# Performance work log

Hardware: AMD Instinct MI355X
Metric: run time of the kernel (lower is better)

The kernel has to match this reference:

```python
import jax, jax.numpy as jnp
import numpy as np
import math

H, D_MODEL, D_C, D_ROPE = 16, 2048, 512, 64
D_HEAD = D_MODEL // H  # 128
D_QK = D_HEAD + D_ROPE  # 192


def precompute_freqs_cis(d_rope, seq_len, base=10000.0):
    # standard RoPE frequencies over pairs -> (seq_len, d_rope//2)
    inv_freq = 1.0 / (base ** (jnp.arange(0, d_rope, 2, dtype=jnp.float32) / d_rope))
    t = jnp.arange(seq_len, dtype=jnp.float32)
    ang = jnp.outer(t, inv_freq)
    return jnp.cos(ang), jnp.sin(ang)


def apply_rotary_emb(x, cos, sin):
    # x: (..., T, d_rope); cos/sin broadcastable (..., T, d_rope//2); interleaved pairs
    x1 = x[..., 0::2]
    x2 = x[..., 1::2]
    r1 = x1 * cos - x2 * sin
    r2 = x1 * sin + x2 * cos
    return jnp.stack([r1, r2], axis=-1).reshape(x.shape)


def setup_inputs() -> dict:
    key = jax.random.key(0)
    ks = jax.random.split(key, 10)
    B, T = 2, 2048
    s = 0.02
    return {
        "query": jax.random.normal(ks[0], (B, T, D_MODEL), jnp.float32),
        "key": jax.random.normal(ks[1], (B, T, D_MODEL), jnp.float32),
        "value": jax.random.normal(ks[2], (B, T, D_MODEL), jnp.float32),
        # weights stored (in_dim, out_dim)
        "W_DKV": jax.random.normal(ks[3], (D_MODEL, D_C), jnp.float32) * s,
        "W_UK": jax.random.normal(ks[4], (D_C, H * D_HEAD), jnp.float32) * s,
        "W_UV": jax.random.normal(ks[5], (D_C, H * D_HEAD), jnp.float32) * s,
        "W_Q": jax.random.normal(ks[6], (D_MODEL, H * D_HEAD), jnp.float32) * s,
        "W_KR": jax.random.normal(ks[7], (D_MODEL, D_ROPE), jnp.float32) * s,
        "W_QR": jax.random.normal(ks[8], (D_MODEL, H * D_ROPE), jnp.float32) * s,
        "W_O": jax.random.normal(ks[9], (H * D_HEAD, D_MODEL), jnp.float32) * s,
    }


def reference(query, key, value, W_DKV, W_UK, W_UV, W_Q, W_KR, W_QR, W_O):
    B, T_q, _ = query.shape
    T_k = key.shape[1]
    # low-rank latent KV compression
    c_kv = key @ W_DKV                                   # (B, Tk, d_c)
    k_nope = (c_kv @ W_UK).reshape(B, T_k, H, D_HEAD).transpose(0, 2, 1, 3)  # bhkd
    v = (c_kv @ W_UV).reshape(B, T_k, H, D_HEAD).transpose(0, 2, 1, 3)       # bhkd
    q_nope = (query @ W_Q).reshape(B, T_q, H, D_HEAD).transpose(0, 2, 1, 3)  # bhqd
    # decoupled RoPE subspace
    k_rope_in = (key @ W_KR)[:, None, :, :]              # (B,1,Tk,d_rope) shared across heads
    q_rope_in = (query @ W_QR).reshape(B, T_q, H, D_ROPE).transpose(0, 2, 1, 3)
    cos_q, sin_q = precompute_freqs_cis(D_ROPE, T_q)
    cos_k, sin_k = precompute_freqs_cis(D_ROPE, T_k)
    q_rope = apply_rotary_emb(q_rope_in, cos_q[None, None], sin_q[None, None])
    k_rope = apply_rotary_emb(k_rope_in, cos_k[None, None], sin_k[None, None])
    k_rope = jnp.broadcast_to(k_rope, (B, H, T_k, D_ROPE))
    # concat content + rope parts
    q = jnp.concatenate([q_nope, q_rope], axis=-1)       # (B,H,Tq,d_qk)
    k = jnp.concatenate([k_nope, k_rope], axis=-1)       # (B,H,Tk,d_qk)
    scores = jnp.einsum('bhqd,bhkd->bhqk', q, k) / math.sqrt(D_QK)
    p_attn = jax.nn.softmax(scores, axis=-1)             # dropout is identity (eval/p=0)
    x = jnp.einsum('bhqk,bhkd->bhqd', p_attn, v)
    x = x.transpose(0, 2, 1, 3).reshape(B, T_q, H * D_HEAD)
    output = x @ W_O
    return output, p_attn
```

## Files before the change

kernel.cpp:

```cpp
#include <hip/hip_runtime.h>
#include <hip/hip_bf16.h>
#include <math.h>

constexpr int B_   = 2;
constexpr int T_   = 2048;
constexpr int DM   = 2048;
constexpr int H_   = 16;
constexpr int DH   = 128;
constexpr int DC   = 512;
constexpr int DR   = 64;
constexpr int DQK  = DH + DR;
constexpr int BT   = B_ * T_;
constexpr int ZBH  = B_ * H_;

typedef __bf16 bf16x8 __attribute__((ext_vector_type(8)));
typedef float  f32x4  __attribute__((ext_vector_type(4)));
typedef unsigned int u32x2 __attribute__((ext_vector_type(2)));
typedef unsigned short u16x4 __attribute__((ext_vector_type(4)));

__device__ __forceinline__ unsigned pk2(float a, float b) {
  __hip_bfloat162 t = __float22bfloat162_rn(make_float2(a, b));
  return *reinterpret_cast<unsigned*>(&t);
}
__device__ __forceinline__ unsigned short bfbits(float v) {
  __hip_bfloat16 t = __float2bfloat16(v);
  return *reinterpret_cast<unsigned short*>(&t);
}

#define WAITVM(N)   asm volatile("s_waitcnt vmcnt(" #N ")" ::: "memory")
#define BARSB() do { __builtin_amdgcn_s_barrier(); __builtin_amdgcn_sched_barrier(0); } while (0)
#define AS1 __attribute__((address_space(1)))
#define AS3 __attribute__((address_space(3)))

__global__ __launch_bounds__(256)
void prep(const float* __restrict__ query, const float* __restrict__ key,
          const float* __restrict__ W_Q, const float* __restrict__ W_QR,
          const float* __restrict__ W_DKV, const float* __restrict__ W_KR,
          const float* __restrict__ W_UK, const float* __restrict__ W_UV,
          const float* __restrict__ W_O,
          __hip_bfloat16* __restrict__ qB, __hip_bfloat16* __restrict__ kB,
          __hip_bfloat16* __restrict__ Wtqall, __hip_bfloat16* __restrict__ Wtkall,
          __hip_bfloat16* __restrict__ Wtkvup, __hip_bfloat16* __restrict__ WtO,
          float* __restrict__ ctab, float* __restrict__ stab) {
  __shared__ float tile[32][33];
  const int blk = blockIdx.x;
  const int tid = threadIdx.x;

  if (blk < 4096) {
    const float* src = (blk < 2048) ? query : key;
    __hip_bfloat16* dst = (blk < 2048) ? qB : kB;
    const long base = (long)(blk & 2047) * 4096;
    #pragma unroll
    for (int c = 0; c < 4; ++c) {
      const long off = base + c * 1024 + tid * 4;
      float4 f = *(const float4*)(src + off);
      u16x4 pk;
      pk[0] = bfbits(f.x); pk[1] = bfbits(f.y); pk[2] = bfbits(f.z); pk[3] = bfbits(f.w);
      *(u16x4*)(dst + off) = pk;
    }
    return;
  }

  int b = blk - 4096;
  const float* W = nullptr; __hip_bfloat16* Wt = nullptr; int K = 2048, N = 2048;
  if (b < 4096)               { W = W_Q;   Wt = Wtqall; }
  else if ((b -= 4096) < 2048){ W = W_QR;  Wt = Wtqall + (size_t)2048 * 2048; N = 1024; }
  else if ((b -= 2048) < 1024){ W = W_DKV; Wt = Wtkall; N = 512; }
  else if ((b -= 1024) < 128) { W = W_KR;  Wt = Wtkall + (size_t)512 * 2048; N = 64; }
  else if ((b -= 128) < 1024) { W = W_UK;  Wt = Wtkvup; K = 512; }
  else if ((b -= 1024) < 1024){ W = W_UV;  Wt = Wtkvup + (size_t)2048 * 512; K = 512; }
  else if ((b -= 1024) < 4096){ W = W_O;   Wt = WtO; }
  else if ((b -= 4096) < 192) {
    float4 z = {0.f, 0.f, 0.f, 0.f};
    *(float4*)((char*)(Wtkall + (size_t)(576 + b) * 2048) + tid * 16) = z;
    return;
  }
  else {
    b -= 192;
    const int i = b * 256 + tid;
    const int t = i >> 5, j = i & 31;
    double inv = pow(10000.0, -(double)j / 32.0);
    double ang = (double)t * inv;
    ctab[i] = (float)cos(ang);
    stab[i] = (float)sin(ang);
    return;
  }
  const int nx = N >> 5;
  const int n0 = (b % nx) << 5, k0 = (b / nx) << 5;
  const int tx = tid & 31, ty = tid >> 5;
  for (int i = ty; i < 32; i += 8)
    tile[i][tx] = W[(long)(k0 + i) * N + n0 + tx];
  __syncthreads();
  for (int i = ty; i < 32; i += 8)
    Wt[(long)(n0 + i) * K + k0 + tx] = __float2bfloat16(tile[tx][i]);
}

template <int MODE>
__global__ __launch_bounds__(256, 2)
void gemm_4w(const __hip_bfloat16* __restrict__ A, const __hip_bfloat16* __restrict__ Bt,
             void* __restrict__ C0, void* __restrict__ C1,
             int M, int N, int K, int lda,
             const float* __restrict__ ctab, const float* __restrict__ stab) {
  const int gnx = N >> 8;
  const int nwg = (M >> 7) * gnx;
  const int cpx = nwg >> 3;
  const int bid = blockIdx.x;
  const int swz = (bid & 7) * cpx + (bid >> 3);
  const int n0 = (swz % gnx) << 8;
  const int m0 = (swz / gnx) << 7;

  __shared__ __align__(16) char lds[73728];

  const int tid  = threadIdx.x;
  const int wc   = tid >> 6;
  const int lane = tid & 63;
  const int rr   = lane & 15;
  const int kq   = lane >> 4;

  const int cs16 = (((tid & 3) ^ ((tid >> 3) & 3)) << 4);
  const int srow = tid >> 2;

  auto stage = [&](int buf, int k0) {
    char* base = lds + buf * 24576;
    #pragma unroll
    for (int c = 0; c < 2; ++c) {
      const char* src = (const char*)A + (((long)(m0 + c * 64 + srow)) * lda + k0) * 2 + cs16;
      __builtin_amdgcn_global_load_lds((const AS1 void*)src,
          (AS3 void*)(base + c * 4096 + tid * 16), 16, 0, 0);
    }
    #pragma unroll
    for (int c = 0; c < 4; ++c) {
      const char* src = (const char*)Bt + (((long)(n0 + c * 64 + srow)) * K + k0) * 2 + cs16;
      __builtin_amdgcn_global_load_lds((const AS1 void*)src,
          (AS3 void*)(base + 8192 + c * 4096 + tid * 16), 16, 0, 0);
    }
  };

  const int g16 = ((kq ^ ((rr >> 1) & 3)) << 4);
  const int aoff0 = rr * 64 + g16;
  const int boff0 = 8192 + (wc * 64 + rr) * 64 + g16;

  f32x4 acc[8][4] = {};

  auto phase = [&](int buf) {
    char* base = lds + buf * 24576;
    bf16x8 a[8], b[4];
    #pragma unroll
    for (int mf = 0; mf < 8; ++mf) a[mf] = *(const bf16x8*)(base + aoff0 + mf * 1024);
    #pragma unroll
    for (int nf = 0; nf < 4; ++nf) b[nf] = *(const bf16x8*)(base + boff0 + nf * 1024);
    __builtin_amdgcn_s_setprio(1);
    #pragma unroll
    for (int mf = 0; mf < 8; ++mf)
      #pragma unroll
      for (int nf = 0; nf < 4; ++nf)
        acc[mf][nf] = __builtin_amdgcn_mfma_f32_16x16x32_bf16(a[mf], b[nf], acc[mf][nf], 0, 0, 0);
    __builtin_amdgcn_s_setprio(0);
  };

  const int NT = K >> 5;
  stage(0, 0); stage(1, 32);
  int cur = 0;
  for (int t = 0; t < NT; ++t) {
    if (t + 2 < NT)       WAITVM(6);
    else if (t + 1 < NT)  WAITVM(6);
    else                  WAITVM(0);
    BARSB();
    if (t + 2 < NT) {
      const int b2 = (cur + 2 >= 3) ? cur - 1 : cur + 2;
      stage(b2, (t + 2) << 5);
    }
    phase(cur);
    cur = (cur + 1 >= 3) ? 0 : cur + 1;
  }

  #pragma unroll
  for (int mf = 0; mf < 8; ++mf) {
    #pragma unroll
    for (int nf = 0; nf < 4; ++nf) {
      const int col = n0 + wc * 64 + nf * 16 + rr;
      const int rbase = m0 + mf * 16 + kq * 4;
      if constexpr (MODE == 1) {
        float* C = (float*)C0;
        #pragma unroll
        for (int j = 0; j < 4; ++j)
          __builtin_nontemporal_store(acc[mf][nf][j], &C[(long)(rbase + j) * N + col]);
      } else if constexpr (MODE == 2) {
        __hip_bfloat16* qall = (__hip_bfloat16*)C0;
        if (col < 2048) {
          #pragma unroll
          for (int j = 0; j < 4; ++j)
            qall[(long)(rbase + j) * 3072 + col] = __float2bfloat16(acc[mf][nf][j]);
        } else {
          const int dr = (col - 2048) & 63;
          const int jj = dr >> 1;
          #pragma unroll
          for (int j = 0; j < 4; ++j) {
            const int row = rbase + j;
            const int t = row & (T_ - 1);
            const float c = ctab[t * 32 + jj], s = stab[t * 32 + jj];
            const float v  = acc[mf][nf][j];
            const float pv = __shfl_xor(v, 1);
            const float res = (dr & 1) ? (pv * s + v * c) : (v * c - pv * s);
            qall[(long)row * 3072 + col] = __float2bfloat16(res);
          }
        }
      } else if constexpr (MODE == 4) {
        __hip_bfloat16* knope = (__hip_bfloat16*)C0;
        __hip_bfloat16* vT    = (__hip_bfloat16*)C1;
        if (col < 2048) {
          #pragma unroll
          for (int j = 0; j < 4; ++j)
            knope[(long)(rbase + j) * 2048 + col] = __float2bfloat16(acc[mf][nf][j]);
        } else {
          const int h = (col - 2048) >> 7, d = (col - 2048) & 127;
          const int z = (rbase >> 11) * 16 + h;
          const int t0 = rbase & (T_ - 1);
          u16x4 pk;
          #pragma unroll
          for (int j = 0; j < 4; ++j) pk[j] = bfbits(acc[mf][nf][j]);
          *(u16x4*)((__hip_bfloat16*)vT + ((long)z * DH + d) * T_ + t0) = pk;
        }
      }
    }
  }
}

template <int MODE>
__global__ __launch_bounds__(512, 2)
void gemm_8w(const __hip_bfloat16* __restrict__ A, const __hip_bfloat16* __restrict__ Bt,
             void* __restrict__ C0, void* __restrict__ C1,
             int M, int N, int K, int lda,
             const float* __restrict__ ctab, const float* __restrict__ stab) {
  const int gnx = N >> 8;
  const int nwg = (M >> 7) * gnx;
  const int cpx = nwg >> 3;
  const int bid = blockIdx.x;
  const int swz = (bid & 7) * cpx + (bid >> 3);
  const int n0 = (swz % gnx) << 8;
  const int m0 = (swz / gnx) << 7;

  __shared__ __align__(16) char lds[147456];

  const int tid  = threadIdx.x;
  const int wv   = tid >> 6;
  const int lane = tid & 63;
  const int wr   = wv >> 2;
  const int wc   = wv & 3;
  const int rr   = lane & 15;
  const int kq   = lane >> 4;

  const int cs16 = (((tid & 3) ^ ((tid >> 3) & 3)) << 4);
  const long arow  = m0 + (tid >> 2);
  const long brow0 = n0 + (tid >> 2);
  const long brow1 = n0 + 128 + (tid >> 2);

  auto stage = [&](int buf, int kh, int k0) {
    char* base = lds + buf * 49152 + kh * 24576;
    const long kk = (long)k0 + kh * 32;
    const char* asrc = (const char*)A + (arow * lda + kk) * 2 + cs16;
    __builtin_amdgcn_global_load_lds((const AS1 void*)asrc,
                                     (AS3 void*)(base + tid * 16), 16, 0, 0);
    const char* bsrc0 = (const char*)Bt + (brow0 * K + kk) * 2 + cs16;
    __builtin_amdgcn_global_load_lds((const AS1 void*)bsrc0,
                                     (AS3 void*)(base + 8192 + tid * 16), 16, 0, 0);
    const char* bsrc1 = (const char*)Bt + (brow1 * K + kk) * 2 + cs16;
    __builtin_amdgcn_global_load_lds((const AS1 void*)bsrc1,
                                     (AS3 void*)(base + 16384 + tid * 16), 16, 0, 0);
  };

  const int g16 = ((kq ^ ((rr >> 1) & 3)) << 4);
  const int aoff0 = (wr * 64 + rr) * 64 + g16;
  const int boff0 = 8192 + (wc * 64 + rr) * 64 + g16;

  f32x4 acc[4][4] = {};

  auto phase = [&](int buf, int kh) {
    char* base = lds + buf * 49152 + kh * 24576;
    bf16x8 a[4], b[4];
    #pragma unroll
    for (int mf = 0; mf < 4; ++mf) a[mf] = *(const bf16x8*)(base + aoff0 + mf * 1024);
    #pragma unroll
    for (int nf = 0; nf < 4; ++nf) b[nf] = *(const bf16x8*)(base + boff0 + nf * 1024);
    __builtin_amdgcn_s_setprio(1);
    #pragma unroll
    for (int mf = 0; mf < 4; ++mf)
      #pragma unroll
      for (int nf = 0; nf < 4; ++nf)
        acc[mf][nf] = __builtin_amdgcn_mfma_f32_16x16x32_bf16(a[mf], b[nf], acc[mf][nf], 0, 0, 0);
    __builtin_amdgcn_s_setprio(0);
  };

  const int NT = K >> 6;
  stage(0, 0, 0); stage(0, 1, 0);
  stage(1, 0, 64); stage(1, 1, 64);
  int cur = 0;
  for (int t = 0; t < NT; ++t) {
    const int b2 = (cur + 2 >= 3) ? cur - 1 : cur + 2;
    if (t + 2 < NT) {
      const int k2 = (t + 2) << 6;
      WAITVM(9);  BARSB();
      stage(b2, 0, k2);
      phase(cur, 0);
      WAITVM(9);  BARSB();
      stage(b2, 1, k2);
      phase(cur, 1);
    } else if (t + 2 == NT) {
      WAITVM(9);  BARSB();  phase(cur, 0);
      WAITVM(6);  BARSB();  phase(cur, 1);
    } else {
      WAITVM(3);  BARSB();  phase(cur, 0);
      WAITVM(0);  BARSB();  phase(cur, 1);
    }
    cur = (cur + 1 >= 3) ? 0 : cur + 1;
  }

  #pragma unroll
  for (int mf = 0; mf < 4; ++mf) {
    #pragma unroll
    for (int nf = 0; nf < 4; ++nf) {
      const int col = n0 + wc * 64 + nf * 16 + rr;
      const int rbase = m0 + wr * 64 + mf * 16 + kq * 4;
      if constexpr (MODE == 3) {
        __hip_bfloat16* ckv = (__hip_bfloat16*)C0;
        __hip_bfloat16* krp = (__hip_bfloat16*)C1;
        if (col < 512) {
          #pragma unroll
          for (int j = 0; j < 4; ++j)
            ckv[(long)(rbase + j) * 512 + col] = __float2bfloat16(acc[mf][nf][j]);
        } else if (col < 576) {
          const int dr = col - 512;
          const int jj = dr >> 1;
          #pragma unroll
          for (int j = 0; j < 4; ++j) {
            const int row = rbase + j;
            const int t = row & (T_ - 1);
            const float c = ctab[t * 32 + jj], s = stab[t * 32 + jj];
            const float v  = acc[mf][nf][j];
            const float pv = __shfl_xor(v, 1);
            const float res = (dr & 1) ? (pv * s + v * c) : (v * c - pv * s);
            krp[(long)row * 64 + dr] = __float2bfloat16(res);
          }
        }
      }
    }
  }
}

__global__ __launch_bounds__(512)
void fused_attn(const __hip_bfloat16* __restrict__ q_all,
                const __hip_bfloat16* __restrict__ knope,
                const __hip_bfloat16* __restrict__ kroper,
                const __hip_bfloat16* __restrict__ vTg,
                float* __restrict__ patt,
                __hip_bfloat16* __restrict__ xplain) {
  constexpr int KT = 64;
  constexpr int NKT = T_ / KT;
  const int bid = blockIdx.x;
  const int swz = (bid & 7) * 64 + (bid >> 3);
  const int z  = swz >> 4;
  const int q0 = (swz & 15) << 7;
  const int b  = z >> 4, h = z & 15;
  const int tid  = threadIdx.x;
  const int wv   = tid >> 6;
  const int lane = tid & 63;
  const int rr   = lane & 15;
  const int kq   = lane >> 4;
  const float scl = 0.0721687836487032f;

  __shared__ __align__(16) char smem[98304];
  char* const lP = smem + 81920;

  const long qrow = (long)(b * T_) + q0 + wv * 16 + rr;
  const __hip_bfloat16* qn = q_all + qrow * 3072 + h * 128;
  const __hip_bfloat16* qr = q_all + qrow * 3072 + 2048 + h * 64;
  bf16x8 qa[6];
  #pragma unroll
  for (int kc = 0; kc < 4; ++kc) qa[kc] = *(const bf16x8*)(qn + kc * 32 + kq * 8);
  #pragma unroll
  for (int kc = 0; kc < 2; ++kc) qa[4 + kc] = *(const bf16x8*)(qr + kc * 32 + kq * 8);

  auto stage_k = [&](char* dst, int kt0) {
    #pragma unroll
    for (int it = 0; it < 3; ++it) {
      const int off = it * 8192 + wv * 1024;
      const int lb  = off + lane * 16;
      const int row = lb / 384, cb = lb % 384;
      const int scb = cb ^ ((row & 7) << 4);
      const long trow = (long)(b * T_) + kt0 + row;
      const char* src = (scb < 256)
          ? (const char*)knope + trow * 4096 + h * 256 + scb
          : (const char*)kroper + trow * 128 + (scb - 256);
      __builtin_amdgcn_global_load_lds((const AS1 void*)src,
          (AS3 void*)(dst + off), 16, 0, 0);
    }
  };
  auto stage_v = [&](char* dst, int kt0) {
    #pragma unroll
    for (int it = 0; it < 2; ++it) {
      const int off = it * 8192 + wv * 1024;
      const int lb  = off + lane * 16;
      const int row = lb >> 7, cb = lb & 127;
      const int scb = cb ^ ((row & 7) << 4);
      const char* src = (const char*)vTg + ((long)(z * DH + row) * T_ + kt0) * 2 + scb;
      __builtin_amdgcn_global_load_lds((const AS1 void*)src,
          (AS3 void*)(dst + off), 16, 0, 0);
    }
  };

  auto qkt = [&](const char* kb0, f32x4 (&sacc)[4]) {
    __builtin_amdgcn_s_setprio(1);
    #pragma unroll
    for (int kc = 0; kc < 6; ++kc) {
      #pragma unroll
      for (int n = 0; n < 4; ++n) {
        const int krow = n * 16 + rr;
        bf16x8 kb = *(const bf16x8*)(kb0 + krow * 384 +
                                     ((kc * 64 + kq * 16) ^ ((krow & 7) << 4)));
        sacc[n] = __builtin_amdgcn_mfma_f32_16x16x32_bf16(kb, qa[kc], sacc[n], 0, 0, 0);
      }
    }
    __builtin_amdgcn_s_setprio(0);
  };

  float srun = 0.f;

  stage_k(smem, 0);
  stage_k(smem + 24576, KT);
  for (int kt = 0; kt < NKT; ++kt) {
    if (kt + 2 < NKT)      { stage_k(smem + ((kt + 2) & 3) * 24576, (kt + 2) * KT); WAITVM(6); }
    else if (kt + 2 == NKT) WAITVM(3);
    else                    WAITVM(0);
    BARSB();
    f32x4 sacc[4] = {};
    qkt(smem + (kt & 3) * 24576, sacc);
    float ts = 0.f;
    #pragma unroll
    for (int n = 0; n < 4; ++n)
      #pragma unroll
      for (int r = 0; r < 4; ++r) ts += __expf(sacc[n][r] * scl);
    ts += __shfl_xor(ts, 16);
    ts += __shfl_xor(ts, 32);
    srun += ts;
  }
  const float pis = 1.f / srun;

  stage_k(smem, 0);
  stage_v(smem + 49152, 0);
  BARSB();

  f32x4 oacc[8] = {};
  const int prow = wv * 16 + rr;
  int cur = 0;
  for (int kt = 0; kt < NKT; ++kt) {
    if (kt == 0) WAITVM(0); else WAITVM(4);
    BARSB();
    if (kt + 1 < NKT) {
      stage_k(smem + (cur ? 0 : 24576), (kt + 1) * KT);
      stage_v(smem + 49152 + (cur ? 0 : 16384), (kt + 1) * KT);
    }
    const char* lK = smem + (cur ? 24576 : 0);
    const char* lV = smem + 49152 + (cur ? 16384 : 0);
    f32x4 sacc[4] = {};
    qkt(lK, sacc);
    const int kt0 = kt * KT;
    #pragma unroll
    for (int n = 0; n < 4; ++n) {
      f32x4 pv;
      #pragma unroll
      for (int r = 0; r < 4; ++r) pv[r] = __expf(sacc[n][r] * scl) * pis;
      __builtin_nontemporal_store(pv,
          (f32x4*)(patt + ((long)z * T_ + q0 + prow) * T_ + kt0 + n * 16 + kq * 4));
      u32x2 pw; pw[0] = pk2(pv[0], pv[1]); pw[1] = pk2(pv[2], pv[3]);
      *(u32x2*)(lP + prow * 128 + ((n * 32 + kq * 8) ^ ((prow & 7) << 4))) = pw;
    }
    bf16x8 pa[2];
    #pragma unroll
    for (int kc = 0; kc < 2; ++kc)
      pa[kc] = *(const bf16x8*)(lP + prow * 128 + ((kc * 64 + kq * 16) ^ ((prow & 7) << 4)));
    __builtin_amdgcn_s_setprio(1);
    #pragma unroll
    for (int kc = 0; kc < 2; ++kc) {
      #pragma unroll
      for (int n = 0; n < 8; ++n) {
        const int vrow = n * 16 + rr;
        bf16x8 vb = *(const bf16x8*)(lV + vrow * 128 + ((kc * 64 + kq * 16) ^ ((vrow & 7) << 4)));
        oacc[n] = __builtin_amdgcn_mfma_f32_16x16x32_bf16(pa[kc], vb, oacc[n], 0, 0, 0);
      }
    }
    __builtin_amdgcn_s_setprio(0);
    cur ^= 1;
  }

  #pragma unroll
  for (int n = 0; n < 8; ++n) {
    #pragma unroll
    for (int r = 0; r < 4; ++r) {
      const int q = q0 + wv * 16 + kq * 4 + r;
      xplain[((long)(b * T_ + q)) * DM + h * DH + n * 16 + rr] = __float2bfloat16(oacc[n][r]);
    }
  }
}

extern "C" void kernel_launch(void* const* d_in, const int* in_sizes, int n_in,
                              void* d_out, int out_size, void* d_ws, size_t ws_size,
                              hipStream_t stream) {
  const float* query = (const float*)d_in[0];
  const float* key   = (const float*)d_in[1];
  const float* W_DKV = (const float*)d_in[3];
  const float* W_UK  = (const float*)d_in[4];
  const float* W_UV  = (const float*)d_in[5];
  const float* W_Q   = (const float*)d_in[6];
  const float* W_KR  = (const float*)d_in[7];
  const float* W_QR  = (const float*)d_in[8];
  const float* W_O   = (const float*)d_in[9];

  float* out  = (float*)d_out;
  float* patt = out + (long)BT * DM;

  char* w = (char*)d_ws;
  auto alloc = [&](size_t bytes) { char* p = w; w += (bytes + 255) & ~(size_t)255; return p; };
  __hip_bfloat16* qB     = (__hip_bfloat16*)alloc((size_t)BT * DM * 2);
  __hip_bfloat16* kB     = (__hip_bfloat16*)alloc((size_t)BT * DM * 2);
  __hip_bfloat16* Wtqall = (__hip_bfloat16*)alloc((size_t)3072 * DM * 2);
  __hip_bfloat16* Wtkall = (__hip_bfloat16*)alloc((size_t)768 * DM * 2);
  __hip_bfloat16* Wtkvup = (__hip_bfloat16*)alloc((size_t)4096 * DC * 2);
  __hip_bfloat16* WtO    = (__hip_bfloat16*)alloc((size_t)DM * DM * 2);
  __hip_bfloat16* q_all  = (__hip_bfloat16*)alloc((size_t)BT * 3072 * 2);
  __hip_bfloat16* ckv    = (__hip_bfloat16*)alloc((size_t)BT * 512 * 2);
  __hip_bfloat16* kroper = (__hip_bfloat16*)alloc((size_t)BT * 64 * 2);
  __hip_bfloat16* knope  = (__hip_bfloat16*)alloc((size_t)BT * 2048 * 2);
  __hip_bfloat16* vT     = (__hip_bfloat16*)alloc((size_t)ZBH * DH * T_ * 2);
  __hip_bfloat16* xplain = (__hip_bfloat16*)alloc((size_t)BT * DM * 2);
  float*          ctab   = (float*)alloc((size_t)T_ * 32 * 4);
  float*          stab   = (float*)alloc((size_t)T_ * 32 * 4);

  prep<<<dim3(17984), 256, 0, stream>>>(
      query, key, W_Q, W_QR, W_DKV, W_KR, W_UK, W_UV, W_O,
      qB, kB, Wtqall, Wtkall, Wtkvup, WtO, ctab, stab);

  gemm_4w<2><<<dim3(384), 256, 0, stream>>>(
      qB, Wtqall, q_all, nullptr, BT, 3072, DM, DM, ctab, stab);
  gemm_8w<3><<<dim3(96), 512, 0, stream>>>(
      kB, Wtkall, ckv, kroper, BT, 768, DM, DM, ctab, stab);
  gemm_4w<4><<<dim3(512), 256, 0, stream>>>(
      ckv, Wtkvup, knope, vT, BT, 4096, DC, 512, nullptr, nullptr);

  fused_attn<<<dim3(512), 512, 0, stream>>>(
      q_all, knope, kroper, vT, patt, xplain);

  gemm_4w<1><<<dim3(256), 256, 0, stream>>>(
      xplain, WtO, out, nullptr, BT, DM, DM, DM, nullptr, nullptr);
}
```

Before: 422.0 us.

## Merge Q and KV down-projection GEMMs into one launch; use 8-wave kernel for output projection

Measured after the change: 401.8 us. 4.8% less time.

```diff
diff --git a/kernel.cpp b/kernel.cpp
--- a/kernel.cpp
+++ b/kernel.cpp
@@ -96,20 +96,17 @@
 }
 
 template <int MODE>
-__global__ __launch_bounds__(256, 2)
-void gemm_4w(const __hip_bfloat16* __restrict__ A, const __hip_bfloat16* __restrict__ Bt,
-             void* __restrict__ C0, void* __restrict__ C1,
-             int M, int N, int K, int lda,
-             const float* __restrict__ ctab, const float* __restrict__ stab) {
+__device__ __forceinline__
+void gemm4w_core(const __hip_bfloat16* __restrict__ A, const __hip_bfloat16* __restrict__ Bt,
+                 void* __restrict__ C0, void* __restrict__ C1,
+                 int N, int K, int lda,
+                 const float* __restrict__ ctab, const float* __restrict__ stab,
+                 int bid, int nwg, char* lds) {
   const int gnx = N >> 8;
-  const int nwg = (M >> 7) * gnx;
   const int cpx = nwg >> 3;
-  const int bid = blockIdx.x;
   const int swz = (bid & 7) * cpx + (bid >> 3);
   const int n0 = (swz % gnx) << 8;
   const int m0 = (swz / gnx) << 7;
-
-  __shared__ __align__(16) char lds[73728];
 
   const int tid  = threadIdx.x;
   const int wc   = tid >> 6;
@@ -162,9 +159,7 @@
   stage(0, 0); stage(1, 32);
   int cur = 0;
   for (int t = 0; t < NT; ++t) {
-    if (t + 2 < NT)       WAITVM(6);
-    else if (t + 1 < NT)  WAITVM(6);
-    else                  WAITVM(0);
+    if (t + 1 < NT) WAITVM(6); else WAITVM(0);
     BARSB();
     if (t + 2 < NT) {
       const int b2 = (cur + 2 >= 3) ? cur - 1 : cur + 2;
@@ -205,6 +200,27 @@
             qall[(long)row * 3072 + col] = __float2bfloat16(res);
           }
         }
+      } else if constexpr (MODE == 3) {
+        __hip_bfloat16* ckv = (__hip_bfloat16*)C0;
+        __hip_bfloat16* krp = (__hip_bfloat16*)C1;
+        if (col < 512) {
+          #pragma unroll
+          for (int j = 0; j < 4; ++j)
+            ckv[(long)(rbase + j) * 512 + col] = __float2bfloat16(acc[mf][nf][j]);
+        } else if (col < 576) {
+          const int dr = col - 512;
+          const int jj = dr >> 1;
+          #pragma unroll
+          for (int j = 0; j < 4; ++j) {
+            const int row = rbase + j;
+            const int t = row & (T_ - 1);
+            const float c = ctab[t * 32 + jj], s = stab[t * 32 + jj];
+            const float v  = acc[mf][nf][j];
+            const float pv = __shfl_xor(v, 1);
+            const float res = (dr & 1) ? (pv * s + v * c) : (v * c - pv * s);
+            krp[(long)row * 64 + dr] = __float2bfloat16(res);
+          }
+        }
       } else if constexpr (MODE == 4) {
         __hip_bfloat16* knope = (__hip_bfloat16*)C0;
         __hip_bfloat16* vT    = (__hip_bfloat16*)C1;
@@ -227,11 +243,34 @@
 }
 
 template <int MODE>
-__global__ __launch_bounds__(512, 2)
-void gemm_8w(const __hip_bfloat16* __restrict__ A, const __hip_bfloat16* __restrict__ Bt,
+__global__ __launch_bounds__(256, 2)
+void gemm_4w(const __hip_bfloat16* __restrict__ A, const __hip_bfloat16* __restrict__ Bt,
              void* __restrict__ C0, void* __restrict__ C1,
              int M, int N, int K, int lda,
              const float* __restrict__ ctab, const float* __restrict__ stab) {
+  __shared__ __align__(16) char lds[73728];
+  gemm4w_core<MODE>(A, Bt, C0, C1, N, K, lda, ctab, stab,
+                    blockIdx.x, (M >> 7) * (N >> 8), lds);
+}
+
+__global__ __launch_bounds__(256, 2)
+void proj_qk(const __hip_bfloat16* __restrict__ qB, const __hip_bfloat16* __restrict__ kB,
+             const __hip_bfloat16* __restrict__ Wtqall, const __hip_bfloat16* __restrict__ Wtkall,
+             __hip_bfloat16* __restrict__ q_all, __hip_bfloat16* __restrict__ ckv,
+             __hip_bfloat16* __restrict__ kroper,
+             const float* __restrict__ ctab, const float* __restrict__ stab) {
+  __shared__ __align__(16) char lds[73728];
+  if (blockIdx.x < 384)
+    gemm4w_core<2>(qB, Wtqall, q_all, nullptr, 3072, 2048, 2048, ctab, stab,
+                   blockIdx.x, 384, lds);
+  else
+    gemm4w_core<3>(kB, Wtkall, ckv, kroper, 768, 2048, 2048, ctab, stab,
+                   blockIdx.x - 384, 96, lds);
+}
+
+__global__ __launch_bounds__(512, 2)
+void gemm_8w_out(const __hip_bfloat16* __restrict__ A, const __hip_bfloat16* __restrict__ Bt,
+                 float* __restrict__ C, int M, int N, int K, int lda) {
   const int gnx = N >> 8;
   const int nwg = (M >> 7) * gnx;
   const int cpx = nwg >> 3;
@@ -321,28 +360,9 @@
     for (int nf = 0; nf < 4; ++nf) {
       const int col = n0 + wc * 64 + nf * 16 + rr;
       const int rbase = m0 + wr * 64 + mf * 16 + kq * 4;
-      if constexpr (MODE == 3) {
-        __hip_bfloat16* ckv = (__hip_bfloat16*)C0;
-        __hip_bfloat16* krp = (__hip_bfloat16*)C1;
-        if (col < 512) {
-          #pragma unroll
-          for (int j = 0; j < 4; ++j)
-            ckv[(long)(rbase + j) * 512 + col] = __float2bfloat16(acc[mf][nf][j]);
-        } else if (col < 576) {
-          const int dr = col - 512;
-          const int jj = dr >> 1;
-          #pragma unroll
-          for (int j = 0; j < 4; ++j) {
-            const int row = rbase + j;
-            const int t = row & (T_ - 1);
-            const float c = ctab[t * 32 + jj], s = stab[t * 32 + jj];
-            const float v  = acc[mf][nf][j];
-            const float pv = __shfl_xor(v, 1);
-            const float res = (dr & 1) ? (pv * s + v * c) : (v * c - pv * s);
-            krp[(long)row * 64 + dr] = __float2bfloat16(res);
-          }
-        }
-      }
+      #pragma unroll
+      for (int j = 0; j < 4; ++j)
+        __builtin_nontemporal_store(acc[mf][nf][j], &C[(long)(rbase + j) * N + col]);
     }
   }
 }
@@ -539,16 +559,15 @@
       query, key, W_Q, W_QR, W_DKV, W_KR, W_UK, W_UV, W_O,
       qB, kB, Wtqall, Wtkall, Wtkvup, WtO, ctab, stab);
 
-  gemm_4w<2><<<dim3(384), 256, 0, stream>>>(
-      qB, Wtqall, q_all, nullptr, BT, 3072, DM, DM, ctab, stab);
-  gemm_8w<3><<<dim3(96), 512, 0, stream>>>(
-      kB, Wtkall, ckv, kroper, BT, 768, DM, DM, ctab, stab);
+  proj_qk<<<dim3(480), 256, 0, stream>>>(
+      qB, kB, Wtqall, Wtkall, q_all, ckv, kroper, ctab, stab);
+
   gemm_4w<4><<<dim3(512), 256, 0, stream>>>(
       ckv, Wtkvup, knope, vT, BT, 4096, DC, 512, nullptr, nullptr);
 
   fused_attn<<<dim3(512), 512, 0, stream>>>(
       q_all, knope, kroper, vT, patt, xplain);
 
-  gemm_4w<1><<<dim3(256), 256, 0, stream>>>(
-      xplain, WtO, out, nullptr, BT, DM, DM, DM, nullptr, nullptr);
-}
+  gemm_8w_out<<<dim3(256), 512, 0, stream>>>(
+      xplain, WtO, out, BT, DM, DM, DM);
+}
```
